# Optimization experiments

Measured on AMD Instinct MI355X. Metric: run time of the kernel, lower is better.

The kernel has to match this reference:

```python
import jax, jax.numpy as jnp
import numpy as np

PI = float(np.pi)


def _make_grid(H, W, stride, k, delta):
    """Gnomonic (tangent-plane) sampling grid for one spherical conv layer.
    Returns rows (Ho, K) and cols (Ho, Wo, K) of fractional pixel coords."""
    Ho, Wo = H // stride, W // stride
    j = jnp.arange(k, dtype=jnp.float32) - (k - 1) / 2.0
    t = jnp.tan(delta / k * j)                      # tangent-plane tap coords
    yy = jnp.repeat(t, k)                           # (K,) vertical
    xx = jnp.tile(t, k)                             # (K,) horizontal
    rho = jnp.sqrt(xx ** 2 + yy ** 2)
    rho_s = jnp.where(rho == 0, 1.0, rho)
    nu = jnp.arctan(rho)
    # latitude of each output row center (equirect: row -> colatitude)
    lat0 = PI / 2 - (jnp.arange(Ho, dtype=jnp.float32) * stride + 0.5) * (PI / H)
    sl, cl = jnp.sin(lat0)[:, None], jnp.cos(lat0)[:, None]   # (Ho,1)
    sn, cn = jnp.sin(nu)[None, :], jnp.cos(nu)[None, :]       # (1,K)
    lat = jnp.arcsin(jnp.clip(cn * sl + (yy[None, :] / rho_s[None, :]) * sn * cl, -1.0, 1.0))
    dlon = jnp.arctan2(xx[None, :] * sn, rho[None, :] * cl * cn - yy[None, :] * sl * sn)
    rows = (PI / 2 - lat) / PI * H - 0.5            # (Ho,K) fractional row
    dcol = dlon / (2 * PI) * W                      # (Ho,K) longitude offset in px
    cols = (jnp.arange(Wo, dtype=jnp.float32) * stride)[None, :, None] + dcol[:, None, :]
    return rows, cols


def _bilinear(x, rows, cols):
    """x: (B,C,H,W); rows (Ho,K); cols (Ho,Wo,K). Latitude clamped, longitude wrapped.
    Returns patches (B,C,Ho,Wo,K)."""
    B, C, H, W = x.shape
    r0 = jnp.floor(rows); wr = (rows - r0)[:, None, :]
    c0 = jnp.floor(cols); wc = cols - c0
    r0i = jnp.clip(r0, 0, H - 1).astype(jnp.int32)
    r1i = jnp.clip(r0 + 1, 0, H - 1).astype(jnp.int32)
    c0i = jnp.mod(c0.astype(jnp.int32), W)
    c1i = jnp.mod(c0i + 1, W)

    def g(ri, ci):
        return x[:, :, ri[:, None, :], ci]          # (B,C,Ho,Wo,K)

    return (g(r0i, c0i) * (1 - wr) * (1 - wc) + g(r0i, c1i) * (1 - wr) * wc
            + g(r1i, c0i) * wr * (1 - wc) + g(r1i, c1i) * wr * wc)


def _sconv(x, w, b, delta, stride):
    k = int(round(np.sqrt(w.shape[-1])))
    rows, cols = _make_grid(x.shape[2], x.shape[3], stride, k, delta)
    p = _bilinear(x, rows, cols)                    # (B,C,Ho,Wo,K)
    return jnp.einsum('bchwk,ock->bohw', p, w) + b[None, :, None, None]


def _bn_relu(x, g, b):
    m = x.mean((0, 2, 3), keepdims=True)
    v = jnp.mean((x - m) ** 2, (0, 2, 3), keepdims=True)  # biased var (torch BN train)
    return jax.nn.relu((x - m) / jnp.sqrt(v + 1e-5) * g[None, :, None, None] + b[None, :, None, None])


def _up2(x):
    return jnp.repeat(jnp.repeat(x, 2, axis=2), 2, axis=3)


def _forward(input, w1, b1, g1, bb1, w2, b2, g2, bb2, w3, b3, g3, bb3,
             w31, b31, g31, bb31, w4, b4, g4, bb4, w41, b41, g41, bb41,
             w5, b5, g5, bb5, w6, b6, g6, bb6):
    x1 = _bn_relu(_sconv(input, w1, b1, PI / 32, 2), g1, bb1)
    x2 = _bn_relu(_sconv(x1, w2, b2, PI / 16, 2), g2, bb2)
    x3 = _bn_relu(_sconv(x2, w3, b3, PI / 4, 2), g3, bb3)
    x31 = _bn_relu(_sconv(x3, w31, b31, PI / 4, 1), g31, bb31)
    x4 = _bn_relu(_sconv(x31, w4, b4, PI / 2, 2), g4, bb4)
    x41 = _bn_relu(_sconv(x4, w41, b41, PI / 2, 1), g41, bb41)
    x5 = _bn_relu(_sconv(jnp.concatenate([_up2(x41), x31], 1), w5, b5, PI / 4, 1), g5, bb5)
    x6 = _bn_relu(_sconv(jnp.concatenate([_up2(x5), x2], 1), w6, b6, PI / 8, 1), g6, bb6)
    return x6


_CFGS = [('1', 32, 6, 7), ('2', 64, 32, 5), ('3', 128, 64, 5), ('31', 128, 128, 3),
         ('4', 256, 128, 3), ('41', 256, 256, 3), ('5', 256, 384, 3), ('6', 128, 320, 3)]


def setup_inputs() -> dict:
    key = jax.random.key(0)
    inp = {'input': jax.random.normal(jax.random.fold_in(key, 0), (4, 6, 256, 512), jnp.float32)}
    for i, (s, o, c, kk) in enumerate(_CFGS):
        kw = jax.random.fold_in(key, i + 1)
        inp['w' + s] = jax.random.normal(kw, (o, c, kk * kk), jnp.float32) / np.float32(np.sqrt(c * kk * kk))
        inp['b' + s] = jnp.zeros((o,), jnp.float32)
        inp['g' + s] = jnp.ones((o,), jnp.float32)
        inp['bb' + s] = jnp.zeros((o,), jnp.float32)
    return inp


def reference(input, w1, b1, g1, bb1, w2, b2, g2, bb2, w3, b3, g3, bb3,
              w31, b31, g31, bb31, w4, b4, g4, bb4, w41, b41, g41, bb41,
              w5, b5, g5, bb5, w6, b6, g6, bb6):
    return _forward(input, w1, b1, g1, bb1, w2, b2, g2, bb2, w3, b3, g3, bb3,
                    w31, b31, g31, bb31, w4, b4, g4, bb4, w41, b41, g41, bb41,
                    w5, b5, g5, bb5, w6, b6, g6, bb6)
```

## Files before the change

kernel.cpp:

```cpp
#include <hip/hip_runtime.h>
#include <cstddef>
#include <cstdint>

#define PI_F 3.14159265358979323846f

typedef __attribute__((ext_vector_type(8))) short short8;
typedef __attribute__((ext_vector_type(4))) float floatx4;

template<int V> struct IC { static constexpr int value = V; };

__device__ __forceinline__ short f2bf(float f) {
    union { float f; unsigned u; } v; v.f = f;
    unsigned r = v.u + 0x7FFFu + ((v.u >> 16) & 1u);
    return (short)(r >> 16);
}

struct WtArgs {
    const float* A[8];
    short* dst[8];
    int M[8], K2[8], C[8], Cp[8], Kp[8];
    int cum[9];
};

__global__ __launch_bounds__(256) void wtrans_all_kernel(WtArgs a)
{
    int g = blockIdx.x * 256 + threadIdx.x;
    if (g >= a.cum[8]) return;
    int L = 0;
#pragma unroll
    for (int i = 1; i < 8; i++) L += (g >= a.cum[i]) ? 1 : 0;
    const int idx = g - a.cum[L];
    const int Kp = a.Kp[L], Cp = a.Cp[L], K2 = a.K2[L], C = a.C[L], M = a.M[L];
    int m = idx / Kp;
    int k = idx - m * Kp;
    int tap = (unsigned)k / (unsigned)Cp;
    int c   = k - tap * Cp;
    float v = 0.f;
    if (m < M && tap < K2 && c < C)
        v = a.A[L][(size_t)m * (C * K2) + c * K2 + tap];
    a.dst[L][idx] = f2bf(v);
}

__global__ __launch_bounds__(256) void zero_kernel(float* __restrict__ p, int n)
{
    int i = blockIdx.x * 256 + threadIdx.x;
    if (i < n) p[i] = 0.f;
}

__global__ __launch_bounds__(256) void zero3_kernel(
    float* __restrict__ a, int na, float* __restrict__ b, int nb,
    float* __restrict__ c, int nc)
{
    int i = blockIdx.x * 256 + threadIdx.x;
    if (i < na) { a[i] = 0.f; return; }
    i -= na;
    if (i < nb) { b[i] = 0.f; return; }
    i -= nb;
    if (i < nc) c[i] = 0.f;
}

#define BNT 64
#define BKT 32
#define LDK 40

template<int MW, int SK, int LGW, int UP, int LGWO, int CS>
__global__ __launch_bounds__(256) void sconv_mfma_kernel(
    const short* __restrict__ Abf,
    const float* __restrict__ src1, const float* __restrict__ src2,
    float2* __restrict__ part, int nBlkN,
    int C1, int Ctot, int Cp, int H, int W, int up1,
    int K2, int ksz, int stride, int lWo, int lHo, float delta,
    float* __restrict__ Y, int M, int Kp, int N, int lgM)
{
    __shared__ short Bs[(LGW != 0) ? 1 : 2][BNT][LDK];
    __shared__ float4 tab[64];
    extern __shared__ __align__(16) char dynLds[];

    constexpr int LGSK = (SK == 1) ? 0 : ((SK == 2) ? 1 : ((SK == 4) ? 2 : 3));

    const int tid = threadIdx.x;
    const int total = gridDim.x;
    const int pid = blockIdx.x;
    const int logical = (pid & 7) * (total >> 3) + (pid >> 3);
    const int mblk = logical & ((1 << lgM) - 1);
    const int rest = logical >> lgM;
    const int kslice = rest & (SK - 1);
    const int nblk = rest >> LGSK;
    const int m0 = mblk * (MW * 64);
    const int n0 = nblk * BNT;

    const int Wo  = 1 << lWo;
    const int Ho  = 1 << lHo;
    const int HW  = 1 << (lWo + lHo);

    const int nHo  = (lWo >= 6) ? 1 : (BNT >> lWo);
    const int nEnt = nHo * K2;
    const int hoBase = (n0 >> lWo) & (Ho - 1);
    if (tid < nEnt) {
        int hoL = tid / K2;
        int i   = tid - hoL * K2;
        int ho_g = hoBase + hoL;
        int jy = i / ksz, jx = i - jy * ksz;
        float halfk = (ksz - 1) * 0.5f;
        float yy = tanf(delta / (float)ksz * ((float)jy - halfk));
        float xx = tanf(delta / (float)ksz * ((float)jx - halfk));
        float rho = sqrtf(xx * xx + yy * yy);
        float rho_s = (rho == 0.f) ? 1.f : rho;
        float nu = atanf(rho);
        float lat0 = PI_F * 0.5f - ((float)(ho_g * stride) + 0.5f) * (PI_F / (float)H);
        float sl = sinf(lat0), cl = cosf(lat0);
        float sn = sinf(nu),  cn = cosf(nu);
        float arg = cn * sl + (yy / rho_s) * sn * cl;
        arg = fminf(1.f, fmaxf(-1.f, arg));
        float lat = asinf(arg);
        float dlon = atan2f(xx * sn, rho * cl * cn - yy * sl * sn);
        float row = (PI_F * 0.5f - lat) / PI_F * (float)H - 0.5f;
        float dcol = dlon / (2.f * PI_F) * (float)W;
        float r0f = floorf(row);
        float fr = row - r0f;
        int r0 = (int)r0f;
        int r0i = min(max(r0, 0), H - 1);
        int r1i = min(max(r0 + 1, 0), H - 1);
        tab[tid] = make_float4(fr, dcol, __int_as_float(r0i), __int_as_float(r1i));
    }

    const int nn    = tid & 63;
    const int kslot = tid >> 6;
    const int n_s  = n0 + nn;
    const int wo_s = n_s & (Wo - 1);
    const int hoL_s = nn >> lWo;
    const int b_s  = n_s >> (lWo + lHo);
    const int tabBase = hoL_s * K2;
    const float wo_px = (float)(wo_s * stride);
    const int Hs = H >> up1, Ws = W >> up1;
    const int plane1 = Hs * Ws;
    const int plane2 = H * W;
    const unsigned boff1 = (unsigned)__builtin_amdgcn_readfirstlane(
        (int)(b_s * C1 * plane1));
    const unsigned boff2 = (unsigned)__builtin_amdgcn_readfirstlane(
        (int)(b_s * (Ctot - C1) * plane2));

    const int Tper = (Kp / BKT) / SK;
    const int t0 = kslice * Tper;
    const bool smallC = (Cp < 32);
    int tap, cb;
    if (smallC) { tap = kslot; cb = 0; }
    else {
        int prog = t0 * BKT;
        tap = prog / Cp;
        cb  = prog - tap * Cp + kslot * 8;
    }
    const int dtap = smallC ? (32 / Cp) : 0;

    const int wave = tid >> 6;
    const int wrow = wave * (MW * 16);
    const int lane = tid & 63;
    const int l16  = lane & 15;
    const int quad = lane >> 4;

    const short* pA[MW];
#pragma unroll
    for (int i = 0; i < MW; i++)
        pA[i] = Abf + (size_t)(m0 + wrow + i * 16 + l16) * Kp + quad * 8;

    floatx4 acc[MW][4];
#pragma unroll
    for (int i = 0; i < MW; i++)
#pragma unroll
        for (int j = 0; j < 4; j++)
            acc[i][j] = (floatx4){0.f, 0.f, 0.f, 0.f};

    if constexpr (LGW == 0) {
        constexpr int CSX = (CS > 0) ? CS : 8;
        struct QS {
            float q00[CSX], q01[CSX], q10[CSX], q11[CSX];
            float w00, w01, w10, w11;
        };
        QS qa, qb;

        auto issueQ = [&](QS& q) {
            const int tapS = __builtin_amdgcn_readfirstlane(tap);
            const int cbS  = __builtin_amdgcn_readfirstlane(cb);
            const int tapc = min(tapS, K2 - 1);
            const float4 e = tab[tabBase + tapc];
            const float fr = e.x;
            const float col = wo_px + e.y;
            const int r0i = __float_as_int(e.z);
            const int r1i = __float_as_int(e.w);
            const float cf = floorf(col);
            const float fc = col - cf;
            const int c0 = ((int)cf) & (W - 1);
            const int c1 = (c0 + 1) & (W - 1);
            const float w11 = fr * fc;
            q.w11 = w11;
            q.w10 = fr - w11;
            q.w01 = fc - w11;
            q.w00 = 1.f - fr - fc + w11;

            const char* sbase; unsigned o00, o01, o10, o11, planeB;
            if (cbS < C1) {
                const int ra = (r0i >> up1) * Ws, rb = (r1i >> up1) * Ws;
                const int ca = c0 >> up1, cx = c1 >> up1;
                const unsigned base = boff1 + (unsigned)cbS * (unsigned)plane1;
                o00 = (base + ra + ca) * 4u; o01 = (base + ra + cx) * 4u;
                o10 = (base + rb + ca) * 4u; o11 = (base + rb + cx) * 4u;
                planeB = (unsigned)plane1 * 4u; sbase = (const char*)src1;
            } else {
                const int ra = r0i * W, rb = r1i * W;
                const unsigned base = boff2 + (unsigned)(cbS - C1) * (unsigned)plane2;
                o00 = (base + ra + c0) * 4u; o01 = (base + ra + c1) * 4u;
                o10 = (base + rb + c0) * 4u; o11 = (base + rb + c1) * 4u;
                planeB = (unsigned)plane2 * 4u; sbase = (const char*)src2;
            }
#pragma unroll
            for (int j = 0; j < CSX; j++) {
                q.q00[j] = *(const float*)(sbase + o00);
                q.q01[j] = *(const float*)(sbase + o01);
                q.q10[j] = *(const float*)(sbase + o10);
                q.q11[j] = *(const float*)(sbase + o11);
                o00 += planeB; o01 += planeB; o10 += planeB; o11 += planeB;
            }
            if (smallC) { tap += dtap; }
            else { cb += 32; if (cb >= Cp) { cb -= Cp; tap++; } }
        };

        auto interpStoreD = [&](const QS& q, int buf) {
            unsigned pk[4];
#pragma unroll
            for (int jj = 0; jj < 4; jj++) {
                if (2 * jj < CSX) {
                    float v0 = q.w00 * q.q00[2 * jj] + q.w01 * q.q01[2 * jj]
                             + q.w10 * q.q10[2 * jj] + q.w11 * q.q11[2 * jj];
                    float v1 = 0.f;
                    if (2 * jj + 1 < CSX)
                        v1 = q.w00 * q.q00[2 * jj + 1] + q.w01 * q.q01[2 * jj + 1]
                           + q.w10 * q.q10[2 * jj + 1] + q.w11 * q.q11[2 * jj + 1];
                    unsigned rr;
                    asm("v_cvt_pk_bf16_f32 %0, %1, %2"
                        : "=v"(rr) : "v"(v0), "v"(v1));
                    pk[jj] = rr;
                } else {
                    pk[jj] = 0u;
                }
            }
            *(uint4*)&Bs[buf][nn][kslot * 8] =
                make_uint4(pk[0], pk[1], pk[2], pk[3]);
        };

        auto mfmaStep = [&](int t) {
            const int k0 = t * BKT;
            const int buf = t & 1;
            short8 af[MW];
#pragma unroll
            for (int i = 0; i < MW; i++)
                af[i] = *(const short8*)(pA[i] + k0);
            short8 bfv[4];
#pragma unroll
            for (int j = 0; j < 4; j++)
                bfv[j] = *(const short8*)&Bs[buf][j * 16 + l16][quad * 8];
#pragma unroll
            for (int i = 0; i < MW; i++)
#pragma unroll
                for (int j = 0; j < 4; j++)
                    acc[i][j] = __builtin_amdgcn_mfma_f32_16x16x32_bf16(
                        af[i], bfv[j], acc[i][j], 0, 0, 0);
        };

        __syncthreads();

        issueQ(qa);
        int t = t0;
        for (; t + 2 <= t0 + Tper; t += 2) {
            issueQ(qb);
            interpStoreD(qa, t & 1);
            __syncthreads();
            mfmaStep(t);
            issueQ(qa);
            interpStoreD(qb, (t + 1) & 1);
            __syncthreads();
            mfmaStep(t + 1);
        }
        if (t < t0 + Tper) {
            interpStoreD(qa, t & 1);
            __syncthreads();
            mfmaStep(t);
        }
    } else {
        constexpr int WC    = 1 << LGW;
        constexpr int LGWS1 = LGW - UP;
        constexpr int NHO   = (LGWO >= 6) ? 1 : (64 >> LGWO);
        constexpr int NHO2  = NHO * 2;
        constexpr int LG2NHO = (NHO == 4) ? 3 : ((NHO == 2) ? 2 : 1);
        constexpr int NU    = 64 * NHO;
        const int kslotU = __builtin_amdgcn_readfirstlane(kslot);

        auto stageTile = [&](int tapT, int cbT) {
            const bool s1 = (cbT < C1);
            const float* srcT = s1 ? src1 : src2;
            const int lgWt = s1 ? LGWS1 : LGW;
            const int upT  = s1 ? UP : 0;
            const int plT  = s1 ? plane1 : plane2;
            const unsigned chB = s1
                ? (boff1 + (unsigned)cbT * (unsigned)plane1)
                : (boff2 + (unsigned)(cbT - C1) * (unsigned)plane2);
            const int tapc2 = min(tapT, K2 - 1);
            const int lgLPU = lgWt - 2;
            const int NIw = (NU << lgWt) >> 10;
            const int uW  = lane >> lgLPU;
            const unsigned colB = (unsigned)(lane & ((1 << lgLPU) - 1)) << 2;
            for (int ii = 0; ii < NIw; ii++) {
                const int idx = kslotU * NIw + ii;
                const int u = (idx << (6 - lgLPU)) + uW;
                const int chL = u >> LG2NHO;
                const int rem = u & (NHO2 - 1);
                const int hoL = rem & (NHO - 1);
                const float4 e = tab[hoL * K2 + tapc2];
                const float rsel = (rem >> (LG2NHO - 1)) ? e.w : e.z;
                const int r = __float_as_int(rsel) >> upT;
                const float* gp = srcT + (chB + (unsigned)chL * (unsigned)plT
                                          + ((unsigned)r << lgWt) + colB);
                __builtin_amdgcn_global_load_lds(
                    (const __attribute__((address_space(1))) void*)gp,
                    (__attribute__((address_space(3))) void*)(dynLds + (size_t)idx * 1024),
                    16, 0, 0);
            }
        };

        int tapS, cb0S;
        {
            int prog = t0 * BKT;
            tapS = prog / Cp;
            cb0S = prog - tapS * Cp;
        }

        __syncthreads();

        stageTile(tapS, cb0S);
        short8 afc[MW];
#pragma unroll
        for (int i2 = 0; i2 < MW; i2++)
            afc[i2] = *(const short8*)(pA[i2] + t0 * BKT);

        for (int t = t0; t < t0 + Tper; t++) {
            tapS = __builtin_amdgcn_readfirstlane(tapS);
            cb0S = __builtin_amdgcn_readfirstlane(cb0S);
            const bool isS1 = (cb0S < C1);
            const int tapcI  = min(tapS, K2 - 1);

            asm volatile("s_waitcnt vmcnt(0)" ::: "memory");
            __syncthreads();

            auto interpStore = [&](auto lgwc, auto upc) {
                constexpr int LGWSRC = decltype(lgwc)::value;
                constexpr int UPX    = decltype(upc)::value;
                constexpr int STEPR  = NHO << LGWSRC;
                constexpr int STEPC  = NHO2 << LGWSRC;
                const float4 e2 = tab[tabBase + tapcI];
                const float fr = e2.x;
                const float col = wo_px + e2.y;
                const float cf = floorf(col);
                const float fc = col - cf;
                const int c0 = ((int)cf) & (WC - 1);
                const int c1 = (c0 + 1) & (WC - 1);
                const int c0s = c0 >> UPX, c1s = c1 >> UPX;
                const float w11 = fr * fc;
                const float w10 = fr - w11;
                const float w01 = fc - w11;
                const float w00 = 1.f - fr - fc + w11;
                const float* rowsF = (const float*)dynLds;
                const float* pc0 = rowsF
                    + ((((kslot * 8) << LG2NHO) + hoL_s) << LGWSRC) + c0s;
                const float* pc1 = pc0 + (c1s - c0s);
                float vv[8];
#pragma unroll
                for (int j = 0; j < 8; j++) {
                    const float x00 = pc0[0];
                    const float x10 = pc0[STEPR];
                    const float x01 = pc1[0];
                    const float x11 = pc1[STEPR];
                    vv[j] = w00 * x00 + w01 * x01 + w10 * x10 + w11 * x11;
                    pc0 += STEPC; pc1 += STEPC;
                }
                unsigned pk[4];
#pragma unroll
                for (int jj = 0; jj < 4; jj++) {
                    unsigned rr;
                    asm("v_cvt_pk_bf16_f32 %0, %1, %2"
                        : "=v"(rr) : "v"(vv[2 * jj]), "v"(vv[2 * jj + 1]));
                    pk[jj] = rr;
                }
                *(uint4*)&Bs[0][nn][kslot * 8] =
                    make_uint4(pk[0], pk[1], pk[2], pk[3]);
            };
            if (isS1) interpStore(IC<LGWS1>{}, IC<UP>{});
            else      interpStore(IC<LGW>{},   IC<0>{});

            __syncthreads();

            int tapN = tapS, cbN = cb0S + BKT;
            if (cbN >= Cp) { cbN = 0; tapN = tapS + 1; }
            const bool more = (t + 1 < t0 + Tper);
            short8 afn[MW];
            if (more) {
#pragma unroll
                for (int i2 = 0; i2 < MW; i2++)
                    afn[i2] = *(const short8*)(pA[i2] + (t + 1) * BKT);
                stageTile(tapN, cbN);
            }

            short8 bfr[4];
#pragma unroll
            for (int j = 0; j < 4; j++)
                bfr[j] = *(const short8*)&Bs[0][j * 16 + l16][quad * 8];
#pragma unroll
            for (int i2 = 0; i2 < MW; i2++)
#pragma unroll
                for (int j = 0; j < 4; j++)
                    acc[i2][j] = __builtin_amdgcn_mfma_f32_16x16x32_bf16(
                        afc[i2], bfr[j], acc[i2][j], 0, 0, 0);

            tapS = tapN; cb0S = cbN;
            if (more) {
#pragma unroll
                for (int i2 = 0; i2 < MW; i2++) afc[i2] = afn[i2];
            }
        }
    }

    if (SK == 1) {
#pragma unroll
        for (int i = 0; i < MW; i++) {
#pragma unroll
            for (int rr = 0; rr < 4; rr++) {
                const int m = m0 + wrow + i * 16 + quad * 4 + rr;
                const bool mv = (m < M);
                float s = 0.f, q = 0.f;
#pragma unroll
                for (int j = 0; j < 4; j++) {
                    const int n = n0 + j * 16 + l16;
                    const float v = acc[i][j][rr];
                    s += v; q += v * v;
                    if (mv) {
                        const int wo = n & (Wo - 1);
                        const int r  = n >> lWo;
                        const int ho = r & (Ho - 1);
                        const int b_ = r >> lHo;
                        Y[((size_t)b_ * M + m) * HW + (ho << lWo) + wo] = v;
                    }
                }
#pragma unroll
                for (int mask = 1; mask < 16; mask <<= 1) {
                    s += __shfl_xor(s, mask);
                    q += __shfl_xor(q, mask);
                }
                if (mv && l16 == 0)
                    part[(size_t)m * nBlkN + nblk] = make_float2(s, q);
            }
        }
    } else {
#pragma unroll
        for (int i = 0; i < MW; i++) {
#pragma unroll
            for (int j = 0; j < 4; j++) {
                const int n = n0 + j * 16 + l16;
                const int wo = n & (Wo - 1);
                const int r  = n >> lWo;
                const int ho = r & (Ho - 1);
                const int b_ = r >> lHo;
#pragma unroll
                for (int rr = 0; rr < 4; rr++) {
                    const int m = m0 + wrow + i * 16 + quad * 4 + rr;
                    if (m < M)
                        unsafeAtomicAdd(
                            &Y[((size_t)b_ * M + m) * HW + (ho << lWo) + wo],
                            acc[i][j][rr]);
                }
            }
        }
    }
}

__global__ __launch_bounds__(256) void bn_stats8_kernel(
    const float* __restrict__ Y, float2* __restrict__ part,
    int Co, int HW, int B)
{
    int co = blockIdx.x;
    int sp = blockIdx.y;
    int tid = threadIdx.x;
    int Nt = B * HW;
    int len = Nt >> 3;
    int start = sp * len, end = start + len;
    float s = 0.f, q = 0.f;
    for (int idx = start + tid; idx < end; idx += 256) {
        int b = idx / HW; int o = idx - b * HW;
        float v = Y[((size_t)b * Co + co) * HW + o];
        s += v; q += v * v;
    }
    __shared__ float sh_s[256], sh_q[256];
    sh_s[tid] = s; sh_q[tid] = q;
    __syncthreads();
    for (int off = 128; off > 0; off >>= 1) {
        if (tid < off) { sh_s[tid] += sh_s[tid + off]; sh_q[tid] += sh_q[tid + off]; }
        __syncthreads();
    }
    if (tid == 0)
        part[co * 8 + sp] = make_float2(sh_s[0], sh_q[0]);
}

__global__ __launch_bounds__(256) void bn_finalize_kernel(
    const float2* __restrict__ part, float2* __restrict__ scSf,
    const float* __restrict__ g, const float* __restrict__ bb,
    int nBlkN, int Nt)
{
    int c = blockIdx.x;
    int tid = threadIdx.x;
    double s = 0.0, q = 0.0;
    for (int k = tid; k < nBlkN; k += 256) {
        float2 p = part[(size_t)c * nBlkN + k];
        s += p.x; q += p.y;
    }
    __shared__ double sh_s[256], sh_q[256];
    sh_s[tid] = s; sh_q[tid] = q;
    __syncthreads();
    for (int off = 128; off > 0; off >>= 1) {
        if (tid < off) { sh_s[tid] += sh_s[tid + off]; sh_q[tid] += sh_q[tid + off]; }
        __syncthreads();
    }
    if (tid == 0) {
        double mean = sh_s[0] / Nt;
        double var = sh_q[0] / Nt - mean * mean;
        if (var < 0.0) var = 0.0;
        float sc = g[c] / sqrtf((float)var + 1e-5f);
        scSf[c] = make_float2(sc, bb[c] - (float)mean * sc);
    }
}

__global__ __launch_bounds__(256) void bn_apply_kernel(
    float* __restrict__ Y, const float2* __restrict__ scSf,
    int Co, int HW, int total)
{
    int idx = blockIdx.x * 256 + threadIdx.x;
    if (idx >= total) return;
    int c = (idx / HW) % Co;
    float2 s = scSf[c];
    float v = Y[idx] * s.x + s.y;
    Y[idx] = v > 0.f ? v : 0.f;
}

__global__ __launch_bounds__(256) void bn_apply_sk_kernel(
    float* __restrict__ Y, const float2* __restrict__ part,
    const float* __restrict__ g, const float* __restrict__ bb,
    int Co, int HW, int Nt, int total)
{
    int idx = blockIdx.x * 256 + threadIdx.x;
    int c = (idx / HW) % Co;
    __shared__ float s_sc, s_sf;
    if (threadIdx.x == 0) {
        double s = 0.0, q = 0.0;
        for (int p = 0; p < 8; p++) {
            float2 pp = part[c * 8 + p];
            s += pp.x; q += pp.y;
        }
        double mean = s / Nt;
        double var = q / Nt - mean * mean;
        if (var < 0.0) var = 0.0;
        float sc = g[c] / sqrtf((float)var + 1e-5f);
        s_sc = sc;
        s_sf = bb[c] - (float)mean * sc;
    }
    __syncthreads();
    if (idx >= total) return;
    float v = Y[idx] * s_sc + s_sf;
    Y[idx] = v > 0.f ? v : 0.f;
}

extern "C" void kernel_launch(void* const* d_in, const int* in_sizes, int n_in,
                              void* d_out, int out_size, void* d_ws, size_t ws_size,
                              hipStream_t stream)
{
    const int B = 4;
    char* ws = (char*)d_ws;
    size_t off = 0;
    auto allocb = [&](size_t bytes) -> void* {
        void* p = ws + off;
        off = (off + bytes + 255) & ~(size_t)255;
        return p;
    };

    float2* part = (float2*)allocb((size_t)65536 * sizeof(float2));
    float2* scSf = (float2*)allocb(256 * sizeof(float2));
    float* x2  = (float*)allocb((size_t)B * 64  * 64 * 128 * 4);
    float* x31 = (float*)allocb((size_t)B * 128 * 32 * 64 * 4);
    float* Q   = (float*)allocb((size_t)B * 32  * 128 * 256 * 4);
    float* x1  = Q;
    float* x3  = Q;
    float* x4  = Q;
    float* x41 = Q + (size_t)B * 256 * 16 * 32;
    float* x5  = Q + 2 * (size_t)B * 256 * 16 * 32;

    static const int kH[8]  = {256, 128,  64,  32,  32,  16,  32,  64};
    static const int kW[8]  = {512, 256, 128,  64,  64,  32,  64, 128};
    static const int kK[8]  = {  7,   5,   5,   3,   3,   3,   3,   3};
    static const int kSt[8] = {  2,   2,   2,   1,   2,   1,   1,   1};
    static const int kC[8]  = {  6,  32,  64, 128, 128, 256, 384, 320};
    static const int kM[8]  = { 32,  64, 128, 128, 256, 256, 256, 128};
    static const int kMW[8] = {  1,   1,   1,   1,   1,   1,   2,   2};
    static const int kSK[8] = {  1,   2,   4,   4,   4,   8,   4,   2};

    int Cp_[8], Kp_[8], Mpad_[8];
    short* Abf[8];
    for (int i = 0; i < 8; i++) {
        int K2 = kK[i] * kK[i];
        int Cp = (kC[i] < 8) ? 8 : kC[i];
        int gran = 32 * kSK[i];
        int Kp = (K2 * Cp + gran - 1) / gran * gran;
        int Mpad = (kM[i] + 63) & ~63;
        Cp_[i] = Cp; Kp_[i] = Kp; Mpad_[i] = Mpad;
        Abf[i] = (short*)allocb((size_t)Mpad * Kp * sizeof(short));
    }
    (void)ws_size; (void)in_sizes; (void)n_in; (void)out_size;

    struct LCfg { const float *s1, *s2; int C1, up; float delta; int widx; float* Y; };
    const float* input = (const float*)d_in[0];
    LCfg L[8] = {
        { input, nullptr,   6, 0, PI_F / 32.f,  1, x1  },
        { x1,    nullptr,  32, 0, PI_F / 16.f,  5, x2  },
        { x2,    nullptr,  64, 0, PI_F / 4.f,   9, x3  },
        { x3,    nullptr, 128, 0, PI_F / 4.f,  13, x31 },
        { x31,   nullptr, 128, 0, PI_F / 2.f,  17, x4  },
        { x4,    nullptr, 256, 0, PI_F / 2.f,  21, x41 },
        { x41,   x31,     256, 1, PI_F / 4.f,  25, x5  },
        { x5,    x2,      256, 1, PI_F / 8.f,  29, (float*)d_out },
    };

    {
        WtArgs wa;
        int cum = 0;
        for (int i = 0; i < 8; i++) {
            wa.A[i]   = (const float*)d_in[L[i].widx];
            wa.dst[i] = Abf[i];
            wa.M[i]   = kM[i];
            wa.K2[i]  = kK[i] * kK[i];
            wa.C[i]   = kC[i];
            wa.Cp[i]  = Cp_[i];
            wa.Kp[i]  = Kp_[i];
            wa.cum[i] = cum;
            cum += Mpad_[i] * Kp_[i];
        }
        wa.cum[8] = cum;
        wtrans_all_kernel<<<dim3((cum + 255) / 256), dim3(256), 0, stream>>>(wa);
    }

    {
        int n_x2 = B * 64 * 64 * 128;
        int n_x31 = B * 128 * 32 * 64;
        int n_out = B * 128 * 64 * 128;
        int tot = n_x2 + n_x31 + n_out;
        zero3_kernel<<<dim3((tot + 255) / 256), dim3(256), 0, stream>>>(
            x2, n_x2, x31, n_x31, (float*)d_out, n_out);
    }

    for (int i = 0; i < 8; i++) {
        const LCfg& c = L[i];
        int H = kH[i], W = kW[i], k = kK[i], st = kSt[i];
        int Ho = H / st, Wo = W / st;
        int K2 = k * k;
        int C  = kC[i], M = kM[i];
        int HW = Ho * Wo;
        int N  = B * HW;
        int lWo = __builtin_ctz(Wo), lHo = __builtin_ctz(Ho);
        const float* gam  = (const float*)d_in[c.widx + 2];
        const float* bet  = (const float*)d_in[c.widx + 3];
        int total = B * M * HW;

        int MWi = kMW[i], SKi = kSK[i];
        int nBlkM = Mpad_[i] / (64 * MWi);
        int nBlkN = N / BNT;
        int totalBlk = nBlkN * nBlkM * SKi;
        int lgM = __builtin_ctz(nBlkM);

        size_t dynB = 0;
        if (i >= 2) {
            int nHo_i = (Wo >= 64) ? 1 : (64 / Wo);
            int w1 = W >> c.up;
            int wmax = c.s2 ? W : w1;
            if (w1 > wmax) wmax = w1;
            dynB = (size_t)(64 * nHo_i) * (size_t)wmax * 4u;
        }

        if (SKi > 1 && i >= 2 && i <= 6 && c.Y != x31)
            zero_kernel<<<dim3((total + 255) / 256), dim3(256), 0, stream>>>(
                c.Y, total);

        #define CONV_ARGS Abf[i], c.s1, c.s2, part, nBlkN, \
            c.C1, C, Cp_[i], H, W, c.up, K2, k, st, lWo, lHo, c.delta, \
            c.Y, M, Kp_[i], N, lgM
        #define LAUNCH(MW_, SK_, LGW_, UP_, LGWO_, CS_, DYN_) \
            sconv_mfma_kernel<MW_,SK_,LGW_,UP_,LGWO_,CS_> \
                <<<dim3(totalBlk), dim3(256), DYN_, stream>>>(CONV_ARGS)
        switch (i) {
            case 0: LAUNCH(1, 1, 0, 0, 0, 6, 0);    break;
            case 1: LAUNCH(1, 2, 0, 0, 0, 0, 0);    break;
            case 2: LAUNCH(1, 4, 7, 0, 6, 0, dynB); break;
            case 3: LAUNCH(1, 4, 6, 0, 6, 0, dynB); break;
            case 4: LAUNCH(1, 4, 6, 0, 5, 0, dynB); break;
            case 5: LAUNCH(1, 8, 5, 0, 5, 0, dynB); break;
            case 6: LAUNCH(2, 4, 6, 1, 6, 0, dynB); break;
            case 7: LAUNCH(2, 2, 7, 1, 7, 0, dynB); break;
        }
        #undef LAUNCH
        #undef CONV_ARGS

        if (SKi > 1) {
            bn_stats8_kernel<<<dim3(M, 8), dim3(256), 0, stream>>>(
                c.Y, part, M, HW, B);
            bn_apply_sk_kernel<<<dim3(total / 256), dim3(256), 0, stream>>>(
                c.Y, part, gam, bet, M, HW, N, total);
        } else {
            bn_finalize_kernel<<<dim3(M), dim3(256), 0, stream>>>(
                part, scSf, gam, bet, nBlkN, N);
            bn_apply_kernel<<<dim3(total / 256), dim3(256), 0, stream>>>(
                c.Y, scSf, M, HW, total);
        }
    }
}
```

Measured before the change: 676.9 us.

## Double-buffer LDS row staging to prefetch next tile before interpolation

Adds a DB template flag that splits the dynamic LDS row buffer into two halves for the src1 path. When both the current and next K-tiles come from src1, the next tile's global_load_lds is issued right after the barrier, before the current tile is interpolated, so global latency overlaps the interpolation and MFMA work. This is enabled for layers 3, 5, 6 and 7, and doubles the dynamic LDS for them, which may lower occupancy.

```diff
diff --git a/kernel.cpp b/kernel.cpp
--- a/kernel.cpp
+++ b/kernel.cpp
@@ -63,7 +63,7 @@
 #define BKT 32
 #define LDK 40
 
-template<int MW, int SK, int LGW, int UP, int LGWO, int CS>
+template<int MW, int SK, int LGW, int UP, int LGWO, int CS, int DB>
 __global__ __launch_bounds__(256) void sconv_mfma_kernel(
     const short* __restrict__ Abf,
     const float* __restrict__ src1, const float* __restrict__ src2,
@@ -292,9 +292,10 @@
         constexpr int NHO2  = NHO * 2;
         constexpr int LG2NHO = (NHO == 4) ? 3 : ((NHO == 2) ? 2 : 1);
         constexpr int NU    = 64 * NHO;
+        constexpr unsigned S1HALF = (unsigned)NU * (1u << LGWS1) * 4u;
         const int kslotU = __builtin_amdgcn_readfirstlane(kslot);
 
-        auto stageTile = [&](int tapT, int cbT) {
+        auto stageTile = [&](int tapT, int cbT, unsigned roff) {
             const bool s1 = (cbT < C1);
             const float* srcT = s1 ? src1 : src2;
             const int lgWt = s1 ? LGWS1 : LGW;
@@ -321,36 +322,53 @@
                                           + ((unsigned)r << lgWt) + colB);
                 __builtin_amdgcn_global_load_lds(
                     (const __attribute__((address_space(1))) void*)gp,
-                    (__attribute__((address_space(3))) void*)(dynLds + (size_t)idx * 1024),
+                    (__attribute__((address_space(3))) void*)
+                        (dynLds + roff + (size_t)idx * 1024),
                     16, 0, 0);
             }
+        };
+
+        auto half1 = [&](int t) -> unsigned {
+            return (DB != 0) ? ((unsigned)(t & 1)) * S1HALF : 0u;
         };
 
         int tapS, cb0S;
         {
             int prog = t0 * BKT;
-            tapS = prog / Cp;
-            cb0S = prog - tapS * Cp;
+            tapS = __builtin_amdgcn_readfirstlane(prog / Cp);
+            cb0S = __builtin_amdgcn_readfirstlane(prog - tapS * Cp);
         }
 
         __syncthreads();
 
-        stageTile(tapS, cb0S);
+        {
+            const bool s1c0 = (cb0S < C1);
+            stageTile(tapS, cb0S, s1c0 ? half1(t0) : 0u);
+        }
         short8 afc[MW];
 #pragma unroll
         for (int i2 = 0; i2 < MW; i2++)
             afc[i2] = *(const short8*)(pA[i2] + t0 * BKT);
 
-        for (int t = t0; t < t0 + Tper; t++) {
+        const int tend = t0 + Tper;
+        for (int t = t0; t < tend; t++) {
             tapS = __builtin_amdgcn_readfirstlane(tapS);
             cb0S = __builtin_amdgcn_readfirstlane(cb0S);
             const bool isS1 = (cb0S < C1);
             const int tapcI  = min(tapS, K2 - 1);
 
+            int tapN = tapS, cbN = cb0S + BKT;
+            if (cbN >= Cp) { cbN = 0; tapN = tapS + 1; }
+            const bool s1N = (cbN < C1);
+            const bool more = (t + 1 < tend);
+
             asm volatile("s_waitcnt vmcnt(0)" ::: "memory");
             __syncthreads();
 
-            auto interpStore = [&](auto lgwc, auto upc) {
+            const bool pre = (DB != 0) && more && isS1 && s1N;
+            if (pre) stageTile(tapN, cbN, half1(t + 1));
+
+            auto interpStore = [&](auto lgwc, auto upc, unsigned roff) {
                 constexpr int LGWSRC = decltype(lgwc)::value;
                 constexpr int UPX    = decltype(upc)::value;
                 constexpr int STEPR  = NHO << LGWSRC;
@@ -367,7 +385,7 @@
                 const float w10 = fr - w11;
                 const float w01 = fc - w11;
                 const float w00 = 1.f - fr - fc + w11;
-                const float* rowsF = (const float*)dynLds;
+                const float* rowsF = (const float*)(dynLds + roff);
                 const float* pc0 = rowsF
                     + ((((kslot * 8) << LG2NHO) + hoL_s) << LGWSRC) + c0s;
                 const float* pc1 = pc0 + (c1s - c0s);
@@ -392,20 +410,17 @@
                 *(uint4*)&Bs[0][nn][kslot * 8] =
                     make_uint4(pk[0], pk[1], pk[2], pk[3]);
             };
-            if (isS1) interpStore(IC<LGWS1>{}, IC<UP>{});
-            else      interpStore(IC<LGW>{},   IC<0>{});
+            if (isS1) interpStore(IC<LGWS1>{}, IC<UP>{}, half1(t));
+            else      interpStore(IC<LGW>{},   IC<0>{},  0u);
 
             __syncthreads();
 
-            int tapN = tapS, cbN = cb0S + BKT;
-            if (cbN >= Cp) { cbN = 0; tapN = tapS + 1; }
-            const bool more = (t + 1 < t0 + Tper);
             short8 afn[MW];
             if (more) {
 #pragma unroll
                 for (int i2 = 0; i2 < MW; i2++)
                     afn[i2] = *(const short8*)(pA[i2] + (t + 1) * BKT);
-                stageTile(tapN, cbN);
+                if (!pre) stageTile(tapN, cbN, s1N ? half1(t + 1) : 0u);
             }
 
             short8 bfr[4];
@@ -680,12 +695,19 @@
         int lgM = __builtin_ctz(nBlkM);
 
         size_t dynB = 0;
+        bool db = (i == 3 || i == 5 || i == 6 || i == 7);
         if (i >= 2) {
             int nHo_i = (Wo >= 64) ? 1 : (64 / Wo);
             int w1 = W >> c.up;
-            int wmax = c.s2 ? W : w1;
-            if (w1 > wmax) wmax = w1;
-            dynB = (size_t)(64 * nHo_i) * (size_t)wmax * 4u;
+            size_t s1half = (size_t)(64 * nHo_i) * (size_t)w1 * 4u;
+            size_t s2B = c.s2 ? (size_t)(64 * nHo_i) * (size_t)W * 4u : 0;
+            if (db) {
+                dynB = 2 * s1half;
+                if (s2B > dynB) dynB = s2B;
+            } else {
+                size_t wmax = c.s2 ? (size_t)W : (size_t)w1;
+                dynB = (size_t)(64 * nHo_i) * wmax * 4u;
+            }
         }
 
         if (SKi > 1 && i >= 2 && i <= 6 && c.Y != x31)
@@ -695,18 +717,18 @@
         #define CONV_ARGS Abf[i], c.s1, c.s2, part, nBlkN, \
             c.C1, C, Cp_[i], H, W, c.up, K2, k, st, lWo, lHo, c.delta, \
             c.Y, M, Kp_[i], N, lgM
-        #define LAUNCH(MW_, SK_, LGW_, UP_, LGWO_, CS_, DYN_) \
-            sconv_mfma_kernel<MW_,SK_,LGW_,UP_,LGWO_,CS_> \
+        #define LAUNCH(MW_, SK_, LGW_, UP_, LGWO_, CS_, DB_, DYN_) \
+            sconv_mfma_kernel<MW_,SK_,LGW_,UP_,LGWO_,CS_,DB_> \
                 <<<dim3(totalBlk), dim3(256), DYN_, stream>>>(CONV_ARGS)
         switch (i) {
-            case 0: LAUNCH(1, 1, 0, 0, 0, 6, 0);    break;
-            case 1: LAUNCH(1, 2, 0, 0, 0, 0, 0);    break;
-            case 2: LAUNCH(1, 4, 7, 0, 6, 0, dynB); break;
-            case 3: LAUNCH(1, 4, 6, 0, 6, 0, dynB); break;
-            case 4: LAUNCH(1, 4, 6, 0, 5, 0, dynB); break;
-            case 5: LAUNCH(1, 8, 5, 0, 5, 0, dynB); break;
-            case 6: LAUNCH(2, 4, 6, 1, 6, 0, dynB); break;
-            case 7: LAUNCH(2, 2, 7, 1, 7, 0, dynB); break;
+            case 0: LAUNCH(1, 1, 0, 0, 0, 6, 0, 0);    break;
+            case 1: LAUNCH(1, 2, 0, 0, 0, 0, 0, 0);    break;
+            case 2: LAUNCH(1, 4, 7, 0, 6, 0, 0, dynB); break;
+            case 3: LAUNCH(1, 4, 6, 0, 6, 0, 1, dynB); break;
+            case 4: LAUNCH(1, 4, 6, 0, 5, 0, 0, dynB); break;
+            case 5: LAUNCH(1, 8, 5, 0, 5, 0, 1, dynB); break;
+            case 6: LAUNCH(2, 4, 6, 1, 6, 0, 1, dynB); break;
+            case 7: LAUNCH(2, 2, 7, 1, 7, 0, 1, dynB); break;
         }
         #undef LAUNCH
         #undef CONV_ARGS
```

Result: no change. 682.1 us (+0.8%).

## Add hybrid staging for last layer: direct register gather for skip-connection channels

Applied to the files above, without the earlier changes.

Adds a HYB template mode used only by the final conv layer. Channels from the upsampled source are still staged into LDS as whole rows, but channels from the full-resolution skip input are gathered directly into registers as four bilinear corners for the next K-step. This shrinks the dynamic LDS footprint to the smaller source's row width and raises that layer's split-K factor from 2 to 4. The cost is more scattered global loads and many more live registers per thread, which may lower occupancy.

```diff
diff --git a/kernel.cpp b/kernel.cpp
--- a/kernel.cpp
+++ b/kernel.cpp
@@ -63,7 +63,7 @@
 #define BKT 32
 #define LDK 40
 
-template<int MW, int SK, int LGW, int UP, int LGWO, int CS>
+template<int MW, int SK, int LGW, int UP, int LGWO, int CS, int HYB>
 __global__ __launch_bounds__(256) void sconv_mfma_kernel(
     const short* __restrict__ Abf,
     const float* __restrict__ src1, const float* __restrict__ src2,
@@ -294,8 +294,12 @@
         constexpr int NU    = 64 * NHO;
         const int kslotU = __builtin_amdgcn_readfirstlane(kslot);
 
+        struct QS2 { float q00[8], q01[8], q10[8], q11[8];
+                     float w00, w01, w10, w11; };
+        QS2 q2;
+
         auto stageTile = [&](int tapT, int cbT) {
-            const bool s1 = (cbT < C1);
+            const bool s1 = HYB ? true : (cbT < C1);
             const float* srcT = s1 ? src1 : src2;
             const int lgWt = s1 ? LGWS1 : LGW;
             const int upT  = s1 ? UP : 0;
@@ -326,22 +330,77 @@
             }
         };
 
+        auto issueQ2 = [&](int tapT, int cbT) {
+            const int tapc = min(tapT, K2 - 1);
+            const float4 e = tab[tabBase + tapc];
+            const float fr = e.x;
+            const float col = wo_px + e.y;
+            const int r0i = __float_as_int(e.z);
+            const int r1i = __float_as_int(e.w);
+            const float cf = floorf(col);
+            const float fc = col - cf;
+            const int c0 = ((int)cf) & (W - 1);
+            const int c1 = (c0 + 1) & (W - 1);
+            const float w11 = fr * fc;
+            q2.w11 = w11;
+            q2.w10 = fr - w11;
+            q2.w01 = fc - w11;
+            q2.w00 = 1.f - fr - fc + w11;
+            const int cc = cbT + kslot * 8 - C1;
+            const unsigned base = boff2 + (unsigned)cc * (unsigned)plane2;
+            const int ra = r0i * W, rb = r1i * W;
+            unsigned o00 = (base + ra + c0) * 4u, o01 = (base + ra + c1) * 4u;
+            unsigned o10 = (base + rb + c0) * 4u, o11 = (base + rb + c1) * 4u;
+            const unsigned planeB = (unsigned)plane2 * 4u;
+            const char* sbase = (const char*)src2;
+#pragma unroll
+            for (int j = 0; j < 8; j++) {
+                q2.q00[j] = *(const float*)(sbase + o00);
+                q2.q01[j] = *(const float*)(sbase + o01);
+                q2.q10[j] = *(const float*)(sbase + o10);
+                q2.q11[j] = *(const float*)(sbase + o11);
+                o00 += planeB; o01 += planeB; o10 += planeB; o11 += planeB;
+            }
+        };
+
+        auto interpStoreQ2 = [&]() {
+            unsigned pk[4];
+#pragma unroll
+            for (int jj = 0; jj < 4; jj++) {
+                float v0 = q2.w00 * q2.q00[2 * jj] + q2.w01 * q2.q01[2 * jj]
+                         + q2.w10 * q2.q10[2 * jj] + q2.w11 * q2.q11[2 * jj];
+                float v1 = q2.w00 * q2.q00[2 * jj + 1] + q2.w01 * q2.q01[2 * jj + 1]
+                         + q2.w10 * q2.q10[2 * jj + 1] + q2.w11 * q2.q11[2 * jj + 1];
+                unsigned rr;
+                asm("v_cvt_pk_bf16_f32 %0, %1, %2"
+                    : "=v"(rr) : "v"(v0), "v"(v1));
+                pk[jj] = rr;
+            }
+            *(uint4*)&Bs[0][nn][kslot * 8] =
+                make_uint4(pk[0], pk[1], pk[2], pk[3]);
+        };
+
         int tapS, cb0S;
         {
             int prog = t0 * BKT;
-            tapS = prog / Cp;
-            cb0S = prog - tapS * Cp;
+            tapS = __builtin_amdgcn_readfirstlane(prog / Cp);
+            cb0S = __builtin_amdgcn_readfirstlane(prog - tapS * Cp);
         }
 
         __syncthreads();
 
-        stageTile(tapS, cb0S);
+        {
+            const bool s1c0 = (cb0S < C1);
+            if (HYB && !s1c0) issueQ2(tapS, cb0S);
+            else              stageTile(tapS, cb0S);
+        }
         short8 afc[MW];
 #pragma unroll
         for (int i2 = 0; i2 < MW; i2++)
             afc[i2] = *(const short8*)(pA[i2] + t0 * BKT);
 
-        for (int t = t0; t < t0 + Tper; t++) {
+        const int tend = t0 + Tper;
+        for (int t = t0; t < tend; t++) {
             tapS = __builtin_amdgcn_readfirstlane(tapS);
             cb0S = __builtin_amdgcn_readfirstlane(cb0S);
             const bool isS1 = (cb0S < C1);
@@ -392,20 +451,27 @@
                 *(uint4*)&Bs[0][nn][kslot * 8] =
                     make_uint4(pk[0], pk[1], pk[2], pk[3]);
             };
-            if (isS1) interpStore(IC<LGWS1>{}, IC<UP>{});
-            else      interpStore(IC<LGW>{},   IC<0>{});
+            if constexpr (HYB) {
+                if (isS1) interpStore(IC<LGWS1>{}, IC<UP>{});
+                else      interpStoreQ2();
+            } else {
+                if (isS1) interpStore(IC<LGWS1>{}, IC<UP>{});
+                else      interpStore(IC<LGW>{},   IC<0>{});
+            }
 
             __syncthreads();
 
             int tapN = tapS, cbN = cb0S + BKT;
             if (cbN >= Cp) { cbN = 0; tapN = tapS + 1; }
-            const bool more = (t + 1 < t0 + Tper);
+            const bool more = (t + 1 < tend);
             short8 afn[MW];
             if (more) {
 #pragma unroll
                 for (int i2 = 0; i2 < MW; i2++)
                     afn[i2] = *(const short8*)(pA[i2] + (t + 1) * BKT);
-                stageTile(tapN, cbN);
+                const bool s1N = (cbN < C1);
+                if (HYB && !s1N) issueQ2(tapN, cbN);
+                else             stageTile(tapN, cbN);
             }
 
             short8 bfr[4];
@@ -605,7 +671,7 @@
     static const int kC[8]  = {  6,  32,  64, 128, 128, 256, 384, 320};
     static const int kM[8]  = { 32,  64, 128, 128, 256, 256, 256, 128};
     static const int kMW[8] = {  1,   1,   1,   1,   1,   1,   2,   2};
-    static const int kSK[8] = {  1,   2,   4,   4,   4,   8,   4,   2};
+    static const int kSK[8] = {  1,   2,   4,   4,   4,   8,   4,   4};
 
     int Cp_[8], Kp_[8], Mpad_[8];
     short* Abf[8];
@@ -683,9 +749,13 @@
         if (i >= 2) {
             int nHo_i = (Wo >= 64) ? 1 : (64 / Wo);
             int w1 = W >> c.up;
-            int wmax = c.s2 ? W : w1;
-            if (w1 > wmax) wmax = w1;
-            dynB = (size_t)(64 * nHo_i) * (size_t)wmax * 4u;
+            if (i == 7) {
+                dynB = (size_t)(64 * nHo_i) * (size_t)w1 * 4u;
+            } else {
+                int wmax = c.s2 ? W : w1;
+                if (w1 > wmax) wmax = w1;
+                dynB = (size_t)(64 * nHo_i) * (size_t)wmax * 4u;
+            }
         }
 
         if (SKi > 1 && i >= 2 && i <= 6 && c.Y != x31)
@@ -695,18 +765,18 @@
         #define CONV_ARGS Abf[i], c.s1, c.s2, part, nBlkN, \
             c.C1, C, Cp_[i], H, W, c.up, K2, k, st, lWo, lHo, c.delta, \
             c.Y, M, Kp_[i], N, lgM
-        #define LAUNCH(MW_, SK_, LGW_, UP_, LGWO_, CS_, DYN_) \
-            sconv_mfma_kernel<MW_,SK_,LGW_,UP_,LGWO_,CS_> \
+        #define LAUNCH(MW_, SK_, LGW_, UP_, LGWO_, CS_, HYB_, DYN_) \
+            sconv_mfma_kernel<MW_,SK_,LGW_,UP_,LGWO_,CS_,HYB_> \
                 <<<dim3(totalBlk), dim3(256), DYN_, stream>>>(CONV_ARGS)
         switch (i) {
-            case 0: LAUNCH(1, 1, 0, 0, 0, 6, 0);    break;
-            case 1: LAUNCH(1, 2, 0, 0, 0, 0, 0);    break;
-            case 2: LAUNCH(1, 4, 7, 0, 6, 0, dynB); break;
-            case 3: LAUNCH(1, 4, 6, 0, 6, 0, dynB); break;
-            case 4: LAUNCH(1, 4, 6, 0, 5, 0, dynB); break;
-            case 5: LAUNCH(1, 8, 5, 0, 5, 0, dynB); break;
-            case 6: LAUNCH(2, 4, 6, 1, 6, 0, dynB); break;
-            case 7: LAUNCH(2, 2, 7, 1, 7, 0, dynB); break;
+            case 0: LAUNCH(1, 1, 0, 0, 0, 6, 0, 0);    break;
+            case 1: LAUNCH(1, 2, 0, 0, 0, 0, 0, 0);    break;
+            case 2: LAUNCH(1, 4, 7, 0, 6, 0, 0, dynB); break;
+            case 3: LAUNCH(1, 4, 6, 0, 6, 0, 0, dynB); break;
+            case 4: LAUNCH(1, 4, 6, 0, 5, 0, 0, dynB); break;
+            case 5: LAUNCH(1, 8, 5, 0, 5, 0, 0, dynB); break;
+            case 6: LAUNCH(2, 4, 6, 1, 6, 0, 0, dynB); break;
+            case 7: LAUNCH(2, 4, 7, 1, 7, 0, 1, dynB); break;
         }
         #undef LAUNCH
         #undef CONV_ARGS
```

Result: slower. 716.8 us (+5.9%).
